# Kernel optimization log

Measured on AMD Instinct MI355X. Metric: run time of the kernel, lower is better.

The kernel has to match this reference:

```python
import jax, jax.numpy as jnp
import numpy as np

NUM_PINS = 10_000_000
NUM_NETS = 3_000_000


def setup_inputs() -> dict:
    key = jax.random.key(0)
    k1, k2 = jax.random.split(key)
    pos = jax.random.normal(k1, (2 * NUM_PINS,), dtype=jnp.float32) * 1000.0
    pin2net_map = jax.random.randint(k2, (NUM_PINS,), 0, NUM_NETS, dtype=jnp.int32)
    net_mask = jnp.ones((NUM_NETS,), dtype=bool)
    return {"pos": pos, "pin2net_map": pin2net_map, "net_mask": net_mask}


def reference(pos, pin2net_map, net_mask):
    # pos: [2*num_pins]; first half = x coords, second half = y coords
    num_pins = pos.shape[0] // 2
    num_nets = net_mask.shape[0]
    x = pos[:num_pins]
    y = pos[num_pins:]

    # per-net bounding box via segment min/max (the atomic scatter reduction)
    xmax = jax.ops.segment_max(x, pin2net_map, num_segments=num_nets)
    xmin = jax.ops.segment_min(x, pin2net_map, num_segments=num_nets)
    ymax = jax.ops.segment_max(y, pin2net_map, num_segments=num_nets)
    ymin = jax.ops.segment_min(y, pin2net_map, num_segments=num_nets)

    # nets with no pins would yield (-inf) - (+inf); mask them out
    counts = jax.ops.segment_sum(jnp.ones_like(x), pin2net_map, num_segments=num_nets)
    valid = net_mask & (counts > 0)

    hpwl_per_net = (xmax - xmin) + (ymax - ymin)
    total = jnp.sum(jnp.where(valid, hpwl_per_net, jnp.float32(0.0)))
    return total.reshape(1)
```

## Files before the change

kernel.cpp:

```cpp
#include <hip/hip_runtime.h>


#define BK_SHIFT 12
#define BK_NETS  4096
#define NBK_MAX  736
#define SUB      4096
#define NSUB     6
#define CHUNK    (SUB * NSUB)
#define TPB      1024
#define RTPB     1024
#define CAP      16384
#define CAP_SHIFT 14

typedef float v4f __attribute__((ext_vector_type(4)));
typedef int   v4i __attribute__((ext_vector_type(4)));

__device__ __forceinline__ unsigned enc(float f) {
    unsigned u = __float_as_uint(f);
    return u ^ ((unsigned)((int)u >> 31) | 0x80000000u);
}
__device__ __forceinline__ float dec(unsigned u) {
    unsigned b = (u & 0x80000000u) ? (u ^ 0x80000000u) : ~u;
    return __uint_as_float(b);
}
__device__ __forceinline__ uint2 pack_rec(float x, float y, int net) {
    unsigned ex = enc(x), ey = enc(y);
    unsigned nl = (unsigned)net & (BK_NETS - 1);
    uint2 r;
    r.x = (ex & ~63u) | (nl >> 6);
    r.y = (ey & ~63u) | (nl & 63u);
    return r;
}

__global__ __launch_bounds__(TPB) void scatter_kernel(
        const float* __restrict__ pos, const int* __restrict__ p2n,
        unsigned* __restrict__ gcur,
        uint2* __restrict__ recs,
        int P, int NBK) {
    __shared__ uint2          stage[SUB];
    __shared__ unsigned short sbk[SUB];
    __shared__ unsigned       hist4[NSUB * NBK_MAX];
    __shared__ unsigned       slab[NBK_MAX];
    __shared__ unsigned       fc[NBK_MAX];
    __shared__ unsigned       sstart[NBK_MAX];
    __shared__ unsigned       scur[NBK_MAX];
    __shared__ unsigned       wsum[TPB / 64];

    const int b = blockIdx.x;
    const int pstart = b * CHUNK;
    const int pcount = min(P - pstart, CHUNK);

    for (int k = threadIdx.x; k < NSUB * NBK_MAX; k += TPB) hist4[k] = 0;
    __syncthreads();

    int nv = pcount >> 2;
    for (int g = threadIdx.x; g < nv; g += TPB) {
        v4i n4 = *(const v4i*)(p2n + pstart + (g << 2));
        unsigned* h = &hist4[(g >> 10) * NBK_MAX];
        atomicAdd(&h[n4.x >> BK_SHIFT], 1u);
        atomicAdd(&h[n4.y >> BK_SHIFT], 1u);
        atomicAdd(&h[n4.z >> BK_SHIFT], 1u);
        atomicAdd(&h[n4.w >> BK_SHIFT], 1u);
    }
    __syncthreads();

    for (int k = threadIdx.x; k < NBK; k += TPB) {
        unsigned c = 0;
        #pragma unroll
        for (int s = 0; s < NSUB; ++s) c += hist4[s * NBK_MAX + k];
        slab[k] = c ? atomicAdd(&gcur[k], c) : 0u;
        fc[k] = 0;
    }
    __syncthreads();

    for (int s = 0; s < NSUB; ++s) {
        int sbase = pstart + s * SUB;
        int scount = min(pcount - s * SUB, SUB);
        if (scount <= 0) break;
        int snv = scount >> 2;
        const unsigned* hs = &hist4[s * NBK_MAX];

        {
            int t = threadIdx.x;
            unsigned v = (t < NBK) ? hs[t] : 0u;
            unsigned x = v;
            #pragma unroll
            for (int off = 1; off < 64; off <<= 1) {
                unsigned y = __shfl_up(x, (unsigned)off);
                if ((t & 63) >= off) x += y;
            }
            if ((t & 63) == 63) wsum[t >> 6] = x;
            __syncthreads();
            if (t < 64) {
                unsigned w = (t < (TPB / 64)) ? wsum[t] : 0u;
                unsigned xx = w;
                #pragma unroll
                for (int off = 1; off < (TPB / 64); off <<= 1) {
                    unsigned y = __shfl_up(xx, (unsigned)off);
                    if (t >= off) xx += y;
                }
                if (t < (TPB / 64)) wsum[t] = xx - w;
            }
            __syncthreads();
            if (t < NBK) {
                unsigned e = x - v + wsum[t >> 6];
                sstart[t] = e;
                scur[t] = e;
            }
            __syncthreads();
        }

        for (int g = threadIdx.x; g < snv; g += TPB) {
            int p = sbase + (g << 2);
            v4i n4 = *(const v4i*)(p2n + p);
            v4f xs = __builtin_nontemporal_load((const v4f*)(pos + p));
            v4f ys = __builtin_nontemporal_load((const v4f*)(pos + P + p));
            int b0 = n4.x >> BK_SHIFT;
            unsigned s0 = atomicAdd(&scur[b0], 1u);
            stage[s0] = pack_rec(xs.x, ys.x, n4.x); sbk[s0] = (unsigned short)b0;
            int b1 = n4.y >> BK_SHIFT;
            unsigned s1 = atomicAdd(&scur[b1], 1u);
            stage[s1] = pack_rec(xs.y, ys.y, n4.y); sbk[s1] = (unsigned short)b1;
            int b2 = n4.z >> BK_SHIFT;
            unsigned s2 = atomicAdd(&scur[b2], 1u);
            stage[s2] = pack_rec(xs.z, ys.z, n4.z); sbk[s2] = (unsigned short)b2;
            int b3 = n4.w >> BK_SHIFT;
            unsigned s3 = atomicAdd(&scur[b3], 1u);
            stage[s3] = pack_rec(xs.w, ys.w, n4.w); sbk[s3] = (unsigned short)b3;
        }
        __syncthreads();

        for (int i = threadIdx.x; i < scount; i += TPB) {
            uint2 r = stage[i];
            int bk = sbk[i];
            unsigned off = slab[bk] + fc[bk] + ((unsigned)i - sstart[bk]);
            if (off < CAP)
                recs[((size_t)bk << CAP_SHIFT) + off] = r;
        }
        __syncthreads();

        for (int k = threadIdx.x; k < NBK; k += TPB) fc[k] += hs[k];
    }
}

__global__ __launch_bounds__(RTPB) void reduce_kernel(
        const uint2* __restrict__ recs,
        const unsigned* __restrict__ gcur,
        const int* __restrict__ mask,
        float* __restrict__ out, int num_nets) {
    int k = blockIdx.x;
    __shared__ unsigned tile[4 * BK_NETS];
    for (int i = threadIdx.x; i < 4 * BK_NETS; i += RTPB) tile[i] = 0;
    __syncthreads();

    unsigned cnt = min(gcur[k], (unsigned)CAP);
    const uint2* base = recs + ((size_t)k << CAP_SHIFT);
    const uint4* b4 = (const uint4*)base;
    unsigned nv = cnt >> 1;
    for (unsigned i = threadIdx.x; i < nv; i += RTPB) {
        uint4 q = b4[i];
        unsigned nl0 = ((q.x & 63u) << 6) | (q.y & 63u);
        unsigned ex0 = q.x & ~63u, ey0 = q.y & ~63u;
        atomicMax(&tile[nl0], ex0);
        atomicMax(&tile[BK_NETS + nl0], (~ex0) & ~63u);
        atomicMax(&tile[2 * BK_NETS + nl0], ey0);
        atomicMax(&tile[3 * BK_NETS + nl0], (~ey0) & ~63u);
        unsigned nl1 = ((q.z & 63u) << 6) | (q.w & 63u);
        unsigned ex1 = q.z & ~63u, ey1 = q.w & ~63u;
        atomicMax(&tile[nl1], ex1);
        atomicMax(&tile[BK_NETS + nl1], (~ex1) & ~63u);
        atomicMax(&tile[2 * BK_NETS + nl1], ey1);
        atomicMax(&tile[3 * BK_NETS + nl1], (~ey1) & ~63u);
    }
    if ((cnt & 1u) && threadIdx.x == 0) {
        uint2 r = base[cnt - 1];
        unsigned nl = ((r.x & 63u) << 6) | (r.y & 63u);
        unsigned ex = r.x & ~63u, ey = r.y & ~63u;
        atomicMax(&tile[nl], ex);
        atomicMax(&tile[BK_NETS + nl], (~ex) & ~63u);
        atomicMax(&tile[2 * BK_NETS + nl], ey);
        atomicMax(&tile[3 * BK_NETS + nl], (~ey) & ~63u);
    }
    __syncthreads();

    int gbase = k << BK_SHIFT;
    int nthis = min(BK_NETS, num_nets - gbase);
    float h = 0.0f;
    for (int n = threadIdx.x; n < nthis; n += RTPB) {
        unsigned a = tile[n];
        if (a != 0u && mask[gbase + n] != 0) {
            float xmax = dec(a);
            float xmin = dec(~tile[BK_NETS + n]);
            float ymax = dec(tile[2 * BK_NETS + n]);
            float ymin = dec(~tile[3 * BK_NETS + n]);
            h += (xmax - xmin) + (ymax - ymin);
        }
    }
    #pragma unroll
    for (int off = 32; off > 0; off >>= 1)
        h += __shfl_down(h, off);
    __syncthreads();
    float* ws = (float*)tile;
    int wid2 = threadIdx.x >> 6;
    if ((threadIdx.x & 63) == 0) ws[wid2] = h;
    __syncthreads();
    if (threadIdx.x == 0) {
        float t = 0.0f;
        #pragma unroll
        for (int w = 0; w < RTPB / 64; ++w) t += ws[w];
        atomicAdd(out, t);
    }
}

__device__ __forceinline__ void upd(unsigned* __restrict__ nets,
                                    float x, float y, int net) {
    unsigned ex = enc(x), ey = enc(y);
    unsigned* base = nets + ((size_t)net << 2);
    atomicMax(base + 0, ex);
    atomicMax(base + 1, ~ex);
    atomicMax(base + 2, ey);
    atomicMax(base + 3, ~ey);
}

__global__ void fb_pin_kernel(const float* __restrict__ pos,
                              const int* __restrict__ p2n,
                              unsigned* __restrict__ nets, int num_pins) {
    int i = blockIdx.x * blockDim.x + threadIdx.x;
    if (i >= num_pins) return;
    upd(nets, pos[i], pos[i + num_pins], p2n[i]);
}

__global__ void fb_net_kernel(const uint4* __restrict__ nets,
                              const int* __restrict__ mask,
                              float* __restrict__ out, int num_nets) {
    int i = blockIdx.x * blockDim.x + threadIdx.x;
    float h = 0.0f;
    if (i < num_nets) {
        uint4 v = nets[i];
        if (v.x != 0u && mask[i] != 0)
            h = (dec(v.x) - dec(~v.y)) + (dec(v.z) - dec(~v.w));
    }
    #pragma unroll
    for (int off = 32; off > 0; off >>= 1)
        h += __shfl_down(h, off);
    __shared__ float s[4];
    int wid = threadIdx.x >> 6;
    if ((threadIdx.x & 63) == 0) s[wid] = h;
    __syncthreads();
    if (threadIdx.x == 0)
        atomicAdd(out, s[0] + s[1] + s[2] + s[3]);
}

extern "C" void kernel_launch(void* const* d_in, const int* in_sizes, int n_in,
                              void* d_out, int out_size, void* d_ws, size_t ws_size,
                              hipStream_t stream) {
    const float* pos = (const float*)d_in[0];
    const int* p2n = (const int*)d_in[1];
    const int* mask = (const int*)d_in[2];
    const int P = in_sizes[0] / 2;
    const int N = in_sizes[2];

    const int NBK = (N + BK_NETS - 1) >> BK_SHIFT;
    const int NB = (P + CHUNK - 1) / CHUNK;

    size_t recs_bytes = (size_t)NBK * CAP * sizeof(uint2);
    size_t need = recs_bytes + (size_t)NBK * sizeof(unsigned) + 256;

    hipMemsetAsync(d_out, 0, sizeof(float), stream);

    size_t mean_load = (NBK > 0) ? (size_t)P / (size_t)NBK : 0;
    size_t slack = 8 * (size_t)(__builtin_sqrt((double)(mean_load + 1))) + 512;
    bool cap_ok = (NBK > 0) && (mean_load + slack <= CAP);

    if (NBK > 0 && NBK <= NBK_MAX && (P & 3) == 0 && ws_size >= need && cap_ok) {
        uint2* recs = (uint2*)d_ws;
        unsigned* gcur = (unsigned*)((char*)d_ws + recs_bytes);
        hipMemsetAsync(gcur, 0, (size_t)NBK * sizeof(unsigned), stream);

        scatter_kernel<<<NB, TPB, 0, stream>>>(pos, p2n, gcur, recs, P, NBK);
        reduce_kernel<<<NBK, RTPB, 0, stream>>>(recs, gcur, mask, (float*)d_out, N);
    } else {
        unsigned* nets = (unsigned*)d_ws;
        hipMemsetAsync(d_ws, 0, (size_t)N * 4 * sizeof(unsigned), stream);
        fb_pin_kernel<<<(P + 255) / 256, 256, 0, stream>>>(pos, p2n, nets, P);
        fb_net_kernel<<<(N + 255) / 256, 256, 0, stream>>>((const uint4*)nets, mask,
                                                           (float*)d_out, N);
    }
}
```

Before: 225.8 us.

## Double net bucket size, reduce x and y in two passes, fold output zeroing

Doubles the nets per bucket to 8192 so there are half as many buckets, and changes the record packing to carry a 13-bit local net id. The reduce kernel now keeps a two-array shared tile and handles x and y in two passes over the records, so a larger bucket fits in LDS. The scatter kernel precomputes a per-bucket write base, which removes one shared read and the separate fc update loop, and it zeroes the output itself instead of using a host memset. The cost is reading each bucket's records twice and fewer reduce blocks, and y coordinates lose one more low bit of precision.

```diff
diff --git a/kernel.cpp b/kernel.cpp
--- a/kernel.cpp
+++ b/kernel.cpp
@@ -1,16 +1,16 @@
 #include <hip/hip_runtime.h>
 
 
-#define BK_SHIFT 12
-#define BK_NETS  4096
-#define NBK_MAX  736
-#define SUB      4096
-#define NSUB     6
+#define BK_SHIFT 13
+#define BK_NETS  8192
+#define NBK_MAX  368
+#define SUB      6144
+#define NSUB     4
 #define CHUNK    (SUB * NSUB)
 #define TPB      1024
 #define RTPB     1024
-#define CAP      16384
-#define CAP_SHIFT 14
+#define CAP      32768
+#define CAP_SHIFT 15
 
 typedef float v4f __attribute__((ext_vector_type(4)));
 typedef int   v4i __attribute__((ext_vector_type(4)));
@@ -27,8 +27,8 @@
     unsigned ex = enc(x), ey = enc(y);
     unsigned nl = (unsigned)net & (BK_NETS - 1);
     uint2 r;
-    r.x = (ex & ~63u) | (nl >> 6);
-    r.y = (ey & ~63u) | (nl & 63u);
+    r.x = (ex & ~63u)  | (nl >> 7);
+    r.y = (ey & ~127u) | (nl & 127u);
     return r;
 }
 
@@ -36,17 +36,19 @@
         const float* __restrict__ pos, const int* __restrict__ p2n,
         unsigned* __restrict__ gcur,
         uint2* __restrict__ recs,
+        float* __restrict__ out,
         int P, int NBK) {
     __shared__ uint2          stage[SUB];
     __shared__ unsigned short sbk[SUB];
     __shared__ unsigned       hist4[NSUB * NBK_MAX];
     __shared__ unsigned       slab[NBK_MAX];
     __shared__ unsigned       fc[NBK_MAX];
-    __shared__ unsigned       sstart[NBK_MAX];
     __shared__ unsigned       scur[NBK_MAX];
+    __shared__ unsigned       wbase[NBK_MAX];
     __shared__ unsigned       wsum[TPB / 64];
 
     const int b = blockIdx.x;
+    if (b == 0 && threadIdx.x == 0) *out = 0.0f;
     const int pstart = b * CHUNK;
     const int pcount = min(P - pstart, CHUNK);
 
@@ -56,7 +58,7 @@
     int nv = pcount >> 2;
     for (int g = threadIdx.x; g < nv; g += TPB) {
         v4i n4 = *(const v4i*)(p2n + pstart + (g << 2));
-        unsigned* h = &hist4[(g >> 10) * NBK_MAX];
+        unsigned* h = &hist4[(g / (SUB >> 2)) * NBK_MAX];
         atomicAdd(&h[n4.x >> BK_SHIFT], 1u);
         atomicAdd(&h[n4.y >> BK_SHIFT], 1u);
         atomicAdd(&h[n4.z >> BK_SHIFT], 1u);
@@ -104,8 +106,9 @@
             __syncthreads();
             if (t < NBK) {
                 unsigned e = x - v + wsum[t >> 6];
-                sstart[t] = e;
                 scur[t] = e;
+                wbase[t] = slab[t] + fc[t] - e;
+                fc[t] += v;
             }
             __syncthreads();
         }
@@ -133,13 +136,11 @@
         for (int i = threadIdx.x; i < scount; i += TPB) {
             uint2 r = stage[i];
             int bk = sbk[i];
-            unsigned off = slab[bk] + fc[bk] + ((unsigned)i - sstart[bk]);
+            unsigned off = wbase[bk] + (unsigned)i;
             if (off < CAP)
                 recs[((size_t)bk << CAP_SHIFT) + off] = r;
         }
         __syncthreads();
-
-        for (int k = threadIdx.x; k < NBK; k += TPB) fc[k] += hs[k];
     }
 }
 
@@ -149,60 +150,75 @@
         const int* __restrict__ mask,
         float* __restrict__ out, int num_nets) {
     int k = blockIdx.x;
-    __shared__ unsigned tile[4 * BK_NETS];
-    for (int i = threadIdx.x; i < 4 * BK_NETS; i += RTPB) tile[i] = 0;
-    __syncthreads();
-
+    __shared__ unsigned tile[2 * BK_NETS];
     unsigned cnt = min(gcur[k], (unsigned)CAP);
-    const uint2* base = recs + ((size_t)k << CAP_SHIFT);
-    const uint4* b4 = (const uint4*)base;
+    const uint4* b4 = (const uint4*)(recs + ((size_t)k << CAP_SHIFT));
     unsigned nv = cnt >> 1;
-    for (unsigned i = threadIdx.x; i < nv; i += RTPB) {
-        uint4 q = b4[i];
-        unsigned nl0 = ((q.x & 63u) << 6) | (q.y & 63u);
-        unsigned ex0 = q.x & ~63u, ey0 = q.y & ~63u;
-        atomicMax(&tile[nl0], ex0);
-        atomicMax(&tile[BK_NETS + nl0], (~ex0) & ~63u);
-        atomicMax(&tile[2 * BK_NETS + nl0], ey0);
-        atomicMax(&tile[3 * BK_NETS + nl0], (~ey0) & ~63u);
-        unsigned nl1 = ((q.z & 63u) << 6) | (q.w & 63u);
-        unsigned ex1 = q.z & ~63u, ey1 = q.w & ~63u;
-        atomicMax(&tile[nl1], ex1);
-        atomicMax(&tile[BK_NETS + nl1], (~ex1) & ~63u);
-        atomicMax(&tile[2 * BK_NETS + nl1], ey1);
-        atomicMax(&tile[3 * BK_NETS + nl1], (~ey1) & ~63u);
-    }
-    if ((cnt & 1u) && threadIdx.x == 0) {
-        uint2 r = base[cnt - 1];
-        unsigned nl = ((r.x & 63u) << 6) | (r.y & 63u);
-        unsigned ex = r.x & ~63u, ey = r.y & ~63u;
-        atomicMax(&tile[nl], ex);
-        atomicMax(&tile[BK_NETS + nl], (~ex) & ~63u);
-        atomicMax(&tile[2 * BK_NETS + nl], ey);
-        atomicMax(&tile[3 * BK_NETS + nl], (~ey) & ~63u);
-    }
-    __syncthreads();
-
     int gbase = k << BK_SHIFT;
     int nthis = min(BK_NETS, num_nets - gbase);
     float h = 0.0f;
+
+    for (int i = threadIdx.x; i < 2 * BK_NETS; i += RTPB) tile[i] = 0;
+    __syncthreads();
+    for (unsigned i = threadIdx.x; i < nv; i += RTPB) {
+        uint4 q = b4[i];
+        unsigned nl0 = ((q.x & 63u) << 7) | (q.y & 127u);
+        unsigned ex0 = q.x & ~63u;
+        atomicMax(&tile[nl0], ex0);
+        atomicMax(&tile[BK_NETS + nl0], (~ex0) & ~63u);
+        unsigned nl1 = ((q.z & 63u) << 7) | (q.w & 127u);
+        unsigned ex1 = q.z & ~63u;
+        atomicMax(&tile[nl1], ex1);
+        atomicMax(&tile[BK_NETS + nl1], (~ex1) & ~63u);
+    }
+    if ((cnt & 1u) && threadIdx.x == 0) {
+        uint2 r = ((const uint2*)b4)[cnt - 1];
+        unsigned nl = ((r.x & 63u) << 7) | (r.y & 127u);
+        unsigned ex = r.x & ~63u;
+        atomicMax(&tile[nl], ex);
+        atomicMax(&tile[BK_NETS + nl], (~ex) & ~63u);
+    }
+    __syncthreads();
     for (int n = threadIdx.x; n < nthis; n += RTPB) {
         unsigned a = tile[n];
-        if (a != 0u && mask[gbase + n] != 0) {
-            float xmax = dec(a);
-            float xmin = dec(~tile[BK_NETS + n]);
-            float ymax = dec(tile[2 * BK_NETS + n]);
-            float ymin = dec(~tile[3 * BK_NETS + n]);
-            h += (xmax - xmin) + (ymax - ymin);
-        }
-    }
+        if (a != 0u && mask[gbase + n] != 0)
+            h += dec(a) - dec(~tile[BK_NETS + n]);
+    }
+    __syncthreads();
+
+    for (int i = threadIdx.x; i < 2 * BK_NETS; i += RTPB) tile[i] = 0;
+    __syncthreads();
+    for (unsigned i = threadIdx.x; i < nv; i += RTPB) {
+        uint4 q = b4[i];
+        unsigned nl0 = ((q.x & 63u) << 7) | (q.y & 127u);
+        unsigned ey0 = q.y & ~127u;
+        atomicMax(&tile[nl0], ey0);
+        atomicMax(&tile[BK_NETS + nl0], (~ey0) & ~127u);
+        unsigned nl1 = ((q.z & 63u) << 7) | (q.w & 127u);
+        unsigned ey1 = q.w & ~127u;
+        atomicMax(&tile[nl1], ey1);
+        atomicMax(&tile[BK_NETS + nl1], (~ey1) & ~127u);
+    }
+    if ((cnt & 1u) && threadIdx.x == 0) {
+        uint2 r = ((const uint2*)b4)[cnt - 1];
+        unsigned nl = ((r.x & 63u) << 7) | (r.y & 127u);
+        unsigned ey = r.y & ~127u;
+        atomicMax(&tile[nl], ey);
+        atomicMax(&tile[BK_NETS + nl], (~ey) & ~127u);
+    }
+    __syncthreads();
+    for (int n = threadIdx.x; n < nthis; n += RTPB) {
+        unsigned a = tile[n];
+        if (a != 0u && mask[gbase + n] != 0)
+            h += dec(a) - dec(~tile[BK_NETS + n]);
+    }
+
     #pragma unroll
     for (int off = 32; off > 0; off >>= 1)
         h += __shfl_down(h, off);
     __syncthreads();
     float* ws = (float*)tile;
-    int wid2 = threadIdx.x >> 6;
-    if ((threadIdx.x & 63) == 0) ws[wid2] = h;
+    if ((threadIdx.x & 63) == 0) ws[threadIdx.x >> 6] = h;
     __syncthreads();
     if (threadIdx.x == 0) {
         float t = 0.0f;
@@ -266,8 +282,6 @@
     size_t recs_bytes = (size_t)NBK * CAP * sizeof(uint2);
     size_t need = recs_bytes + (size_t)NBK * sizeof(unsigned) + 256;
 
-    hipMemsetAsync(d_out, 0, sizeof(float), stream);
-
     size_t mean_load = (NBK > 0) ? (size_t)P / (size_t)NBK : 0;
     size_t slack = 8 * (size_t)(__builtin_sqrt((double)(mean_load + 1))) + 512;
     bool cap_ok = (NBK > 0) && (mean_load + slack <= CAP);
@@ -277,10 +291,12 @@
         unsigned* gcur = (unsigned*)((char*)d_ws + recs_bytes);
         hipMemsetAsync(gcur, 0, (size_t)NBK * sizeof(unsigned), stream);
 
-        scatter_kernel<<<NB, TPB, 0, stream>>>(pos, p2n, gcur, recs, P, NBK);
+        scatter_kernel<<<NB, TPB, 0, stream>>>(pos, p2n, gcur, recs,
+                                               (float*)d_out, P, NBK);
         reduce_kernel<<<NBK, RTPB, 0, stream>>>(recs, gcur, mask, (float*)d_out, N);
     } else {
         unsigned* nets = (unsigned*)d_ws;
+        hipMemsetAsync(d_out, 0, sizeof(float), stream);
         hipMemsetAsync(d_ws, 0, (size_t)N * 4 * sizeof(unsigned), stream);
         fb_pin_kernel<<<(P + 255) / 256, 256, 0, stream>>>(pos, p2n, nets, P);
         fb_net_kernel<<<(N + 255) / 256, 256, 0, stream>>>((const uint4*)nets, mask,
```

New measurement: 219.7 us. -2.7%, faster.
